# Kernel tuning notes

Hardware: AMD Instinct MI355X
Metric: run time of the kernel (lower is better)

## Reference

```python
import jax, jax.numpy as jnp
import numpy as np


def _norm(graph):
    # graph: [B, N, N]. degree = row sums; inv degree with nan/inf -> 0;
    # diag_embed+bmm in the original is exactly row-wise broadcast scaling.
    degree = jnp.sum(graph, axis=2)                 # [B, N]
    inv = 1.0 / degree
    inv = jnp.where(jnp.isfinite(inv), inv, 0.0)    # remove_nan_inf
    return graph * inv[:, :, None]                  # [B, N, N]


def setup_inputs() -> dict:
    key = jax.random.key(0)
    # list of 2 batched adjacency tensors, stacked on leading axis
    adj = jax.random.uniform(key, (2, 32, 1024, 1024), dtype=jnp.float32)
    return {"adj": adj}


def reference(adj) -> jnp.ndarray:
    # vmap over the "list" axis; returns [L, B, N, N]
    return jax.vmap(_norm)(adj)
```

## Files before the change

kernel.cpp:

```cpp
#include <hip/hip_runtime.h>

__global__ __launch_bounds__(256) void
normalizer_kernel(const float* __restrict__ in, float* __restrict__ out) {
    const size_t row = blockIdx.x;
    const float4* __restrict__ rin  = reinterpret_cast<const float4*>(in  + row * 1024);
    float4* __restrict__       rout = reinterpret_cast<float4*>      (out + row * 1024);

    float4 v = rin[threadIdx.x];

    float s = (v.x + v.y) + (v.z + v.w);

    #pragma unroll
    for (int off = 32; off > 0; off >>= 1)
        s += __shfl_down(s, off, 64);

    __shared__ float wsum[4];
    const int wave = threadIdx.x >> 6;
    const int lane = threadIdx.x & 63;
    if (lane == 0) wsum[wave] = s;
    __syncthreads();

    const float total = (wsum[0] + wsum[1]) + (wsum[2] + wsum[3]);
    float inv = 1.0f / total;
    if (!isfinite(inv)) inv = 0.0f;

    v.x *= inv; v.y *= inv; v.z *= inv; v.w *= inv;
    rout[threadIdx.x] = v;
}

extern "C" void kernel_launch(void* const* d_in, const int* in_sizes, int n_in,
                              void* d_out, int out_size, void* d_ws, size_t ws_size,
                              hipStream_t stream) {
    const float* adj = reinterpret_cast<const float*>(d_in[0]);
    float* out = reinterpret_cast<float*>(d_out);
    const int n_rows = in_sizes[0] / 1024;
    normalizer_kernel<<<dim3(n_rows), dim3(256), 0, stream>>>(adj, out);
}
```

Baseline: 412.0 us.

## Assign one wave per row and drop block-level shared-memory reduction

Each 64-lane wave now handles a whole 1024-float row with four float4 loads per lane, and reduces with an xor butterfly so every lane holds the sum. This removes the shared-memory exchange and block barrier and raises per-thread memory-level parallelism, with a quarter as many blocks. The floating-point summation order changes slightly, and the grid assumes the row count is divisible by four.

```diff
diff --git a/kernel.cpp b/kernel.cpp
--- a/kernel.cpp
+++ b/kernel.cpp
@@ -2,30 +2,38 @@
 
 __global__ __launch_bounds__(256) void
 normalizer_kernel(const float* __restrict__ in, float* __restrict__ out) {
-    const size_t row = blockIdx.x;
+    const int lane = threadIdx.x & 63;
+    const int wave = threadIdx.x >> 6;
+    const size_t row = (size_t)blockIdx.x * 4 + wave;
+
     const float4* __restrict__ rin  = reinterpret_cast<const float4*>(in  + row * 1024);
     float4* __restrict__       rout = reinterpret_cast<float4*>      (out + row * 1024);
 
-    float4 v = rin[threadIdx.x];
+    float4 v0 = rin[lane];
+    float4 v1 = rin[lane + 64];
+    float4 v2 = rin[lane + 128];
+    float4 v3 = rin[lane + 192];
 
-    float s = (v.x + v.y) + (v.z + v.w);
+    float s01 = ((v0.x + v0.y) + (v0.z + v0.w)) + ((v1.x + v1.y) + (v1.z + v1.w));
+    float s23 = ((v2.x + v2.y) + (v2.z + v2.w)) + ((v3.x + v3.y) + (v3.z + v3.w));
+    float s = s01 + s23;
 
     #pragma unroll
     for (int off = 32; off > 0; off >>= 1)
-        s += __shfl_down(s, off, 64);
+        s += __shfl_xor(s, off, 64);
 
-    __shared__ float wsum[4];
-    const int wave = threadIdx.x >> 6;
-    const int lane = threadIdx.x & 63;
-    if (lane == 0) wsum[wave] = s;
-    __syncthreads();
-
-    const float total = (wsum[0] + wsum[1]) + (wsum[2] + wsum[3]);
-    float inv = 1.0f / total;
+    float inv = 1.0f / s;
     if (!isfinite(inv)) inv = 0.0f;
 
-    v.x *= inv; v.y *= inv; v.z *= inv; v.w *= inv;
-    rout[threadIdx.x] = v;
+    v0.x *= inv; v0.y *= inv; v0.z *= inv; v0.w *= inv;
+    v1.x *= inv; v1.y *= inv; v1.z *= inv; v1.w *= inv;
+    v2.x *= inv; v2.y *= inv; v2.z *= inv; v2.w *= inv;
+    v3.x *= inv; v3.y *= inv; v3.z *= inv; v3.w *= inv;
+
+    rout[lane]       = v0;
+    rout[lane + 64]  = v1;
+    rout[lane + 128] = v2;
+    rout[lane + 192] = v3;
 }
 
 extern "C" void kernel_launch(void* const* d_in, const int* in_sizes, int n_in,
@@ -34,5 +42,5 @@
     const float* adj = reinterpret_cast<const float*>(d_in[0]);
     float* out = reinterpret_cast<float*>(d_out);
     const int n_rows = in_sizes[0] / 1024;
-    normalizer_kernel<<<dim3(n_rows), dim3(256), 0, stream>>>(adj, out);
+    normalizer_kernel<<<dim3(n_rows / 4), dim3(256), 0, stream>>>(adj, out);
 }
```

Result: slower. 424.7 us (+3.1%).
